# Optimization experiments

Hardware: AMD Instinct MI355X
Metric: run time of the kernel (lower is better)

## Reference

```python
import jax, jax.numpy as jnp
import numpy as np


def setup_inputs() -> dict:
    key = jax.random.key(0)
    ks = jax.random.split(key, 6)
    B, T, U = 4, 160, 80
    De, Dd = 640, 640
    inner, vocab = 640, 1024
    return {
        "enc_state": jax.random.normal(ks[0], (B, T, De), jnp.float32),
        "dec_state": jax.random.normal(ks[1], (B, U, Dd), jnp.float32),
        "W1": jax.random.normal(ks[2], (De + Dd, inner), jnp.float32) * (1.0 / np.sqrt(De + Dd)),
        "b1": jax.random.normal(ks[3], (inner,), jnp.float32) * 0.02,
        "W2": jax.random.normal(ks[4], (inner, vocab), jnp.float32) * (1.0 / np.sqrt(inner)),
        "b2": jax.random.normal(ks[5], (vocab,), jnp.float32) * 0.02,
    }


def reference(enc_state, dec_state, W1, b1, W2, b2):
    # Faithful to: cat([enc tiled over U, dec tiled over T], -1) @ W1 + b1,
    # algebraically split so the [B,T,U,2D] concat is never materialized:
    # cat(e, d) @ W1 == e @ W1[:De] + d @ W1[De:]
    De = enc_state.shape[-1]
    W1_enc, W1_dec = W1[:De], W1[De:]
    enc_proj = jnp.einsum("btd,dh->bth", enc_state, W1_enc)   # [B,T,H]
    dec_proj = jnp.einsum("bud,dh->buh", dec_state, W1_dec)   # [B,U,H]
    # broadcast add over the (T,U) lattice -> [B,T,U,H]
    hidden = jnp.tanh(enc_proj[:, :, None, :] + dec_proj[:, None, :, :] + b1)
    logits = jnp.einsum("btuh,hv->btuv", hidden, W2) + b2     # [B,T,U,V]
    return logits
```

## Files before the change

### kernel.cpp

```cpp
#include <hip/hip_runtime.h>
#include <hip/hip_bf16.h>
#include <cstdint>

#define D_    640
#define V_    1024
#define M_    51200

typedef __bf16 bf16x8 __attribute__((ext_vector_type(8)));
typedef float floatx4 __attribute__((ext_vector_type(4)));

__device__ __forceinline__ void g2l16(const void* g, void* l) {
    __builtin_amdgcn_global_load_lds((const __attribute__((address_space(1))) void*)g,
                                     (__attribute__((address_space(3))) void*)l,
                                     16, 0, 0);
}

__device__ __forceinline__ float fast_tanh(float x) {
    float e = __builtin_amdgcn_exp2f(x * 2.8853900817779268f);
    return 1.0f - 2.0f * __builtin_amdgcn_rcpf(e + 1.0f);
}

__global__ __launch_bounds__(256) void proj_kernel(
    const float* __restrict__ enc, const float* __restrict__ dec,
    const float* __restrict__ W1, const float* __restrict__ b1,
    float* __restrict__ encp, float* __restrict__ decp) {
    __shared__ float As[64][36];
    __shared__ float Ws[32][68];

    const int rt = blockIdx.y;
    const int ct = blockIdx.x;
    const bool is_enc = (rt < 10);
    const float* Asrc; const float* Wsrc; float* Cdst;
    if (is_enc) { Asrc = enc + (size_t)rt * 64 * D_;        Wsrc = W1;           Cdst = encp + (size_t)rt * 64 * D_; }
    else        { Asrc = dec + (size_t)(rt - 10) * 64 * D_; Wsrc = W1 + D_ * D_; Cdst = decp + (size_t)(rt - 10) * 64 * D_; }

    const int tid = threadIdx.x;
    const int ar = tid >> 2,  ac = (tid & 3) * 8;
    const int wr2 = tid >> 3, wc2 = (tid & 7) * 8;
    const int tr = tid >> 4,  tc = tid & 15;

    float acc[4][4] = {};
    for (int k0 = 0; k0 < D_; k0 += 32) {
        __syncthreads();
        *(floatx4*)&As[ar][ac]       = *(const floatx4*)&Asrc[(size_t)ar * D_ + k0 + ac];
        *(floatx4*)&As[ar][ac + 4]   = *(const floatx4*)&Asrc[(size_t)ar * D_ + k0 + ac + 4];
        *(floatx4*)&Ws[wr2][wc2]     = *(const floatx4*)&Wsrc[(size_t)(k0 + wr2) * D_ + ct * 64 + wc2];
        *(floatx4*)&Ws[wr2][wc2 + 4] = *(const floatx4*)&Wsrc[(size_t)(k0 + wr2) * D_ + ct * 64 + wc2 + 4];
        __syncthreads();
#pragma unroll
        for (int kk = 0; kk < 32; kk++) {
            floatx4 w = *(const floatx4*)&Ws[kk][tc * 4];
            float a0 = As[tr * 4 + 0][kk], a1 = As[tr * 4 + 1][kk];
            float a2 = As[tr * 4 + 2][kk], a3 = As[tr * 4 + 3][kk];
#pragma unroll
            for (int j = 0; j < 4; j++) {
                acc[0][j] += a0 * w[j]; acc[1][j] += a1 * w[j];
                acc[2][j] += a2 * w[j]; acc[3][j] += a3 * w[j];
            }
        }
    }
    floatx4 bv = {0.f, 0.f, 0.f, 0.f};
    if (is_enc) bv = *(const floatx4*)&b1[ct * 64 + tc * 4];
#pragma unroll
    for (int i = 0; i < 4; i++) {
        floatx4 v = { acc[i][0] + bv[0], acc[i][1] + bv[1],
                      acc[i][2] + bv[2], acc[i][3] + bv[3] };
        *(floatx4*)&Cdst[(size_t)(tr * 4 + i) * D_ + ct * 64 + tc * 4] = v;
    }
}

__global__ __launch_bounds__(256) void w2t_kernel(
    const float* __restrict__ W2, __bf16* __restrict__ W2t) {
    __shared__ __bf16 tile[32][33];
    const int vt = blockIdx.x;
    const int kt = blockIdx.y;
    const int tx = threadIdx.x & 31, ty = threadIdx.x >> 5;
#pragma unroll
    for (int i = 0; i < 4; i++)
        tile[ty + i * 8][tx] = (__bf16)W2[(size_t)(kt * 32 + ty + i * 8) * V_ + vt * 32 + tx];
    __syncthreads();
#pragma unroll
    for (int i = 0; i < 4; i++)
        W2t[(size_t)(vt * 32 + ty + i * 8) * D_ + kt * 32 + tx] = tile[tx][ty + i * 8];
}

__global__ __launch_bounds__(256) void hidden_kernel(
    const float* __restrict__ encp, const float* __restrict__ decp,
    __bf16* __restrict__ H) {
    const unsigned g = blockIdx.x * 256u + threadIdx.x;
    const unsigned row = g / 80u;
    const unsigned hg  = g % 80u;
    const unsigned u   = row % 80u;
    const unsigned bt  = row / 80u;
    const unsigned b   = bt / 160u;

    const float* ep = encp + (size_t)bt * D_ + hg * 8;
    const float* dp = decp + (size_t)(b * 80u + u) * D_ + hg * 8;

    floatx4 e0 = *(const floatx4*)ep, e1 = *(const floatx4*)(ep + 4);
    floatx4 d0 = *(const floatx4*)dp, d1 = *(const floatx4*)(dp + 4);

    bf16x8 hv;
#pragma unroll
    for (int i = 0; i < 4; i++) hv[i]     = (__bf16)fast_tanh(e0[i] + d0[i]);
#pragma unroll
    for (int i = 0; i < 4; i++) hv[i + 4] = (__bf16)fast_tanh(e1[i] + d1[i]);

    *(bf16x8*)(H + (size_t)g * 8) = hv;
}

__global__ __launch_bounds__(256, 2) void gemm_kernel(
    const __bf16* __restrict__ H, const __bf16* __restrict__ W2t,
    const float* __restrict__ b2, float* __restrict__ C) {
    __shared__ __align__(128) char lds[49152];

    const int bid = blockIdx.x;
    const int swz = (bid & 7) * 200 + (bid >> 3);
    const int mt = swz >> 2, nt = swz & 3;
    const int m0 = mt * 128, n0 = nt * 256;

    const int tid = threadIdx.x;
    const int w = tid >> 6, l = tid & 63;
    const int lr = l & 15, lk = l >> 4;

    char* ldsp = (char*)lds;

    const int srow = tid >> 2;
    const int sphy = tid & 3;
    const unsigned scol = (unsigned)((sphy ^ ((srow >> 1) & 3)) * 16);
    const char* Ag = (const char*)H   + (size_t)(m0 + srow) * 1280 + scol;
    const char* Bg = (const char*)W2t + (size_t)(n0 + srow) * 1280 + scol;
    const unsigned sdst = (unsigned)tid * 16u;

    const unsigned px16 = (unsigned)((lk ^ ((lr >> 1) & 3)) * 16);

    floatx4 accT[4][8] = {};

#define STAGE_A(BUF, T) do { \
    g2l16(Ag + (T) * 64,          ldsp + (BUF) * 8192 + sdst); \
    g2l16(Ag + 81920 + (T) * 64,  ldsp + (BUF) * 8192 + sdst + 4096); \
  } while (0)
#define STAGE_B(BUF, T) do { \
    g2l16(Bg + (T) * 64,           ldsp + 16384 + (BUF) * 16384 + sdst); \
    g2l16(Bg +  81920 + (T) * 64,  ldsp + 16384 + (BUF) * 16384 + sdst + 4096); \
    g2l16(Bg + 163840 + (T) * 64,  ldsp + 16384 + (BUF) * 16384 + sdst + 8192); \
    g2l16(Bg + 245760 + (T) * 64,  ldsp + 16384 + (BUF) * 16384 + sdst + 12288); \
  } while (0)

#define FRAGS_MFMA(BUF) do { \
    bf16x8 af[8], bfr[4]; \
    _Pragma("unroll") for (int i = 0; i < 8; ++i) \
        af[i] = *(const bf16x8*)(ldsp + (BUF) * 8192 + (i * 16 + lr) * 64 + px16); \
    _Pragma("unroll") for (int j = 0; j < 4; ++j) \
        bfr[j] = *(const bf16x8*)(ldsp + 16384 + (BUF) * 16384 + (w * 64 + j * 16 + lr) * 64 + px16); \
    _Pragma("unroll") for (int j = 0; j < 4; ++j) \
        _Pragma("unroll") for (int i = 0; i < 8; ++i) \
            accT[j][i] = __builtin_amdgcn_mfma_f32_16x16x32_bf16(bfr[j], af[i], accT[j][i], 0, 0, 0); \
  } while (0)

    STAGE_A(0, 0); STAGE_B(0, 0);
    __syncthreads();

#pragma unroll 1
    for (int t = 0; t < 20; ++t) {
        const int buf = t & 1, nb = buf ^ 1;
        if (t < 19) { STAGE_A(nb, t + 1); STAGE_B(nb, t + 1); }
        FRAGS_MFMA(buf);
        __syncthreads();
    }

#pragma unroll
    for (int j = 0; j < 4; ++j) {
        const int col0 = n0 + w * 64 + j * 16 + lk * 4;
        const floatx4 bv = *(const floatx4*)&b2[col0];
#pragma unroll
        for (int i = 0; i < 8; ++i) {
            const int row = m0 + i * 16 + lr;
            floatx4 v = { accT[j][i][0] + bv[0], accT[j][i][1] + bv[1],
                          accT[j][i][2] + bv[2], accT[j][i][3] + bv[3] };
            *(floatx4*)&C[(size_t)row * V_ + col0] = v;
        }
    }
#undef STAGE_A
#undef STAGE_B
#undef FRAGS_MFMA
}

extern "C" void kernel_launch(void* const* d_in, const int* in_sizes, int n_in,
                              void* d_out, int out_size, void* d_ws, size_t ws_size,
                              hipStream_t stream) {
    const float* enc = (const float*)d_in[0];
    const float* dec = (const float*)d_in[1];
    const float* W1  = (const float*)d_in[2];
    const float* b1  = (const float*)d_in[3];
    const float* W2  = (const float*)d_in[4];
    const float* b2  = (const float*)d_in[5];
    float* out = (float*)d_out;

    char* ws = (char*)d_ws;
    float*  encp = (float*)ws;
    float*  decp = (float*)(ws + 1638400);
    __bf16* W2t  = (__bf16*)(ws + 1638400 + 819200);
    __bf16* Hbuf = (__bf16*)(ws + 1638400 + 819200 + 1310720);

    proj_kernel<<<dim3(10, 15), 256, 0, stream>>>(enc, dec, W1, b1, encp, decp);
    w2t_kernel<<<dim3(32, 20), 256, 0, stream>>>(W2, W2t);
    hidden_kernel<<<16000, 256, 0, stream>>>(encp, decp, Hbuf);
    gemm_kernel<<<1600, 256, 0, stream>>>(Hbuf, W2t, b2, out);
}
```

Measured before the change: 355.9 us.

## Fuse tanh hidden production into GEMM and tile full vocab per block

```diff
diff --git a/kernel.cpp b/kernel.cpp
--- a/kernel.cpp
+++ b/kernel.cpp
@@ -84,106 +84,102 @@
         W2t[(size_t)(vt * 32 + ty + i * 8) * D_ + kt * 32 + tx] = tile[tx][ty + i * 8];
 }
 
-__global__ __launch_bounds__(256) void hidden_kernel(
+__global__ __launch_bounds__(512, 2) void joint_kernel(
     const float* __restrict__ encp, const float* __restrict__ decp,
-    __bf16* __restrict__ H) {
-    const unsigned g = blockIdx.x * 256u + threadIdx.x;
-    const unsigned row = g / 80u;
-    const unsigned hg  = g % 80u;
-    const unsigned u   = row % 80u;
-    const unsigned bt  = row / 80u;
-    const unsigned b   = bt / 160u;
-
-    const float* ep = encp + (size_t)bt * D_ + hg * 8;
-    const float* dp = decp + (size_t)(b * 80u + u) * D_ + hg * 8;
-
-    floatx4 e0 = *(const floatx4*)ep, e1 = *(const floatx4*)(ep + 4);
-    floatx4 d0 = *(const floatx4*)dp, d1 = *(const floatx4*)(dp + 4);
-
-    bf16x8 hv;
-#pragma unroll
-    for (int i = 0; i < 4; i++) hv[i]     = (__bf16)fast_tanh(e0[i] + d0[i]);
-#pragma unroll
-    for (int i = 0; i < 4; i++) hv[i + 4] = (__bf16)fast_tanh(e1[i] + d1[i]);
-
-    *(bf16x8*)(H + (size_t)g * 8) = hv;
-}
-
-__global__ __launch_bounds__(256, 2) void gemm_kernel(
-    const __bf16* __restrict__ H, const __bf16* __restrict__ W2t,
-    const float* __restrict__ b2, float* __restrict__ C) {
-    __shared__ __align__(128) char lds[49152];
+    const __bf16* __restrict__ W2t, const float* __restrict__ b2,
+    float* __restrict__ C) {
+    __shared__ __align__(128) char lds[73728];
 
     const int bid = blockIdx.x;
-    const int swz = (bid & 7) * 200 + (bid >> 3);
-    const int mt = swz >> 2, nt = swz & 3;
-    const int m0 = mt * 128, n0 = nt * 256;
+    const int swz = (bid & 7) * 100 + (bid >> 3);
+    const int m0 = swz * 64;
 
     const int tid = threadIdx.x;
     const int w = tid >> 6, l = tid & 63;
     const int lr = l & 15, lk = l >> 4;
 
     char* ldsp = (char*)lds;
-
-    const int srow = tid >> 2;
-    const int sphy = tid & 3;
-    const unsigned scol = (unsigned)((sphy ^ ((srow >> 1) & 3)) * 16);
-    const char* Ag = (const char*)H   + (size_t)(m0 + srow) * 1280 + scol;
-    const char* Bg = (const char*)W2t + (size_t)(n0 + srow) * 1280 + scol;
-    const unsigned sdst = (unsigned)tid * 16u;
+    char* ldsB = ldsp + 8192;
+
+    const char* WbL = (const char*)W2t
+        + (size_t)(w * 16 + (l >> 2)) * 1280
+        + (unsigned)((((l & 3) ^ ((l >> 3) & 3)) * 16));
+    const unsigned bdst = (unsigned)(w * 1024 + l * 16);
+
+    const int pr = (tid & 255) >> 2;
+    const int kq = tid & 3;
+    const int R  = m0 + pr;
+    const int bt = R / 80;
+    const int uu = R - bt * 80;
+    const int drw = (bt / 160) * 80 + uu;
+    const float* ep = encp + (size_t)bt * D_ + kq * 8;
+    const float* dp = decp + (size_t)drw * D_ + kq * 8;
+    const unsigned pwr = (unsigned)(pr * 64 + (((kq ^ ((pr >> 1) & 3)) * 16)));
 
     const unsigned px16 = (unsigned)((lk ^ ((lr >> 1) & 3)) * 16);
 
-    floatx4 accT[4][8] = {};
-
-#define STAGE_A(BUF, T) do { \
-    g2l16(Ag + (T) * 64,          ldsp + (BUF) * 8192 + sdst); \
-    g2l16(Ag + 81920 + (T) * 64,  ldsp + (BUF) * 8192 + sdst + 4096); \
+    floatx4 accT[8][4] = {};
+
+#define STAGE_B(T) do { \
+    const char* _s = WbL + (size_t)(T) * 64; \
+    _Pragma("unroll") for (int c = 0; c < 8; ++c) \
+        g2l16(_s + (size_t)c * 163840, ldsB + bdst + c * 8192); \
   } while (0)
-#define STAGE_B(BUF, T) do { \
-    g2l16(Bg + (T) * 64,           ldsp + 16384 + (BUF) * 16384 + sdst); \
-    g2l16(Bg +  81920 + (T) * 64,  ldsp + 16384 + (BUF) * 16384 + sdst + 4096); \
-    g2l16(Bg + 163840 + (T) * 64,  ldsp + 16384 + (BUF) * 16384 + sdst + 8192); \
-    g2l16(Bg + 245760 + (T) * 64,  ldsp + 16384 + (BUF) * 16384 + sdst + 12288); \
-  } while (0)
-
-#define FRAGS_MFMA(BUF) do { \
-    bf16x8 af[8], bfr[4]; \
-    _Pragma("unroll") for (int i = 0; i < 8; ++i) \
-        af[i] = *(const bf16x8*)(ldsp + (BUF) * 8192 + (i * 16 + lr) * 64 + px16); \
-    _Pragma("unroll") for (int j = 0; j < 4; ++j) \
-        bfr[j] = *(const bf16x8*)(ldsp + 16384 + (BUF) * 16384 + (w * 64 + j * 16 + lr) * 64 + px16); \
-    _Pragma("unroll") for (int j = 0; j < 4; ++j) \
-        _Pragma("unroll") for (int i = 0; i < 8; ++i) \
-            accT[j][i] = __builtin_amdgcn_mfma_f32_16x16x32_bf16(bfr[j], af[i], accT[j][i], 0, 0, 0); \
-  } while (0)
-
-    STAGE_A(0, 0); STAGE_B(0, 0);
+
+#define PRODUCE_A(BUF, T) do { \
+    if (tid < 256) { \
+      const float* _e = ep + (T) * 32; const float* _d = dp + (T) * 32; \
+      floatx4 e0 = *(const floatx4*)_e, e1 = *(const floatx4*)(_e + 4); \
+      floatx4 d0 = *(const floatx4*)_d, d1 = *(const floatx4*)(_d + 4); \
+      bf16x8 h; \
+      _Pragma("unroll") for (int i2 = 0; i2 < 4; ++i2) { \
+        h[i2]     = (__bf16)fast_tanh(e0[i2] + d0[i2]); \
+        h[i2 + 4] = (__bf16)fast_tanh(e1[i2] + d1[i2]); \
+      } \
+      *(bf16x8*)(ldsp + (BUF) * 4096 + pwr) = h; \
+    } } while (0)
+
+    STAGE_B(0);
+    PRODUCE_A(0, 0);
     __syncthreads();
 
 #pragma unroll 1
     for (int t = 0; t < 20; ++t) {
         const int buf = t & 1, nb = buf ^ 1;
-        if (t < 19) { STAGE_A(nb, t + 1); STAGE_B(nb, t + 1); }
-        FRAGS_MFMA(buf);
+        bf16x8 af[4], bfr[8];
+#pragma unroll
+        for (int i = 0; i < 4; ++i)
+            af[i] = *(const bf16x8*)(ldsp + buf * 4096 + (i * 16 + lr) * 64 + px16);
+#pragma unroll
+        for (int j = 0; j < 8; ++j)
+            bfr[j] = *(const bf16x8*)(ldsB + (w * 128 + j * 16 + lr) * 64 + px16);
         __syncthreads();
-    }
-
-#pragma unroll
-    for (int j = 0; j < 4; ++j) {
-        const int col0 = n0 + w * 64 + j * 16 + lk * 4;
+        if (t < 19) {
+            STAGE_B(t + 1);
+            PRODUCE_A(nb, t + 1);
+        }
+#pragma unroll
+        for (int j = 0; j < 8; ++j)
+#pragma unroll
+            for (int i = 0; i < 4; ++i)
+                accT[j][i] = __builtin_amdgcn_mfma_f32_16x16x32_bf16(bfr[j], af[i], accT[j][i], 0, 0, 0);
+        if (t < 19) __syncthreads();
+    }
+
+#pragma unroll
+    for (int j = 0; j < 8; ++j) {
+        const int col0 = w * 128 + j * 16 + lk * 4;
         const floatx4 bv = *(const floatx4*)&b2[col0];
 #pragma unroll
-        for (int i = 0; i < 8; ++i) {
+        for (int i = 0; i < 4; ++i) {
             const int row = m0 + i * 16 + lr;
             floatx4 v = { accT[j][i][0] + bv[0], accT[j][i][1] + bv[1],
                           accT[j][i][2] + bv[2], accT[j][i][3] + bv[3] };
             *(floatx4*)&C[(size_t)row * V_ + col0] = v;
         }
     }
-#undef STAGE_A
 #undef STAGE_B
-#undef FRAGS_MFMA
+#undef PRODUCE_A
 }
 
 extern "C" void kernel_launch(void* const* d_in, const int* in_sizes, int n_in,
@@ -201,10 +197,8 @@
     float*  encp = (float*)ws;
     float*  decp = (float*)(ws + 1638400);
     __bf16* W2t  = (__bf16*)(ws + 1638400 + 819200);
-    __bf16* Hbuf = (__bf16*)(ws + 1638400 + 819200 + 1310720);
 
     proj_kernel<<<dim3(10, 15), 256, 0, stream>>>(enc, dec, W1, b1, encp, decp);
     w2t_kernel<<<dim3(32, 20), 256, 0, stream>>>(W2, W2t);
-    hidden_kernel<<<16000, 256, 0, stream>>>(encp, decp, Hbuf);
-    gemm_kernel<<<1600, 256, 0, stream>>>(Hbuf, W2t, b2, out);
-}
+    joint_kernel<<<800, 512, 0, stream>>>(encp, decp, W2t, b2, out);
+}
```

Result: slower. 394.7 us (+10.9%).
